# Optimization experiments

Measured on AMD Instinct MI355X. Metric: run time of the kernel, lower is better.

The kernel has to match this reference:

```python
import jax, jax.numpy as jnp
import numpy as np

HIDDEN = 768
HEADS = 12
HEAD_DIM = HIDDEN // HEADS


def setup_inputs() -> dict:
    key = jax.random.key(0)
    ks = jax.random.split(key, 6)
    B, N = 32, 577  # N = 1 CLS + 576 patches
    x = jax.random.normal(ks[0], (B, N, HIDDEN), dtype=jnp.float32)
    seg_bias = jax.random.uniform(ks[1], (B, N - 1), dtype=jnp.float32)
    w_qkv = jax.random.normal(ks[2], (HIDDEN, 3 * HIDDEN), dtype=jnp.float32) * 0.02
    b_qkv = jnp.zeros((3 * HIDDEN,), dtype=jnp.float32)
    w_proj = jax.random.normal(ks[3], (HIDDEN, HIDDEN), dtype=jnp.float32) * 0.02
    b_proj = jnp.zeros((HIDDEN,), dtype=jnp.float32)
    seg_scale = jnp.ones((), dtype=jnp.float32)
    return {"x": x, "seg_bias": seg_bias, "w_qkv": w_qkv, "b_qkv": b_qkv,
            "w_proj": w_proj, "b_proj": b_proj, "seg_scale": seg_scale}


def reference(x, seg_bias, w_qkv, b_qkv, w_proj, b_proj, seg_scale):
    B, N, _ = x.shape
    scale = HEAD_DIM ** -0.5
    qkv = x @ w_qkv + b_qkv                       # (B, N, 3*H*D)
    qkv = qkv.reshape(B, N, 3, HEADS, HEAD_DIM)
    q = qkv[:, :, 0].transpose(0, 2, 1, 3)        # (B, H, N, D)
    k = qkv[:, :, 1].transpose(0, 2, 1, 3)
    v = qkv[:, :, 2].transpose(0, 2, 1, 3)
    attn = jnp.einsum('bhqd,bhkd->bhqk', q, k) * scale  # (B, H, N, N)
    # additive seg bias on CLS-query row, patch keys only (cols 1:)
    bias = (seg_bias * seg_scale)[:, None, None, :]     # (B,1,1,N-1)
    attn = attn.at[:, :, 0:1, 1:].add(bias)
    attn = jax.nn.softmax(attn, axis=-1)
    out = jnp.einsum('bhqk,bhkd->bhqd', attn, v)        # (B, H, N, D)
    out = out.transpose(0, 2, 1, 3).reshape(B, N, HIDDEN)
    return out @ w_proj + b_proj
```

## Files before the change

kernel.cpp:

```cpp
#include <hip/hip_runtime.h>


typedef unsigned short bf16_t;
typedef __attribute__((ext_vector_type(8))) short short8;
typedef __attribute__((ext_vector_type(4))) short short4v;
typedef __attribute__((ext_vector_type(4))) float f32x4;

#define B_    32
#define N_    577
#define BN_   18464
#define HID_  768
#define NH_   12
#define HD_   64
#define QKVC_ 2304
#define NPAD_ 640
#define PB_LD 68

__device__ __forceinline__ bf16_t f2bf(float f) {
  union { float f; unsigned u; } x; x.f = f;
  unsigned r = x.u + 0x7fffu + ((x.u >> 16) & 1u);
  return (bf16_t)(r >> 16);
}

__device__ __forceinline__ unsigned cvt_pk_bf16(float a, float b) {
  unsigned r;
  asm("v_cvt_pk_bf16_f32 %0, %1, %2" : "=v"(r) : "v"(a), "v"(b));
  return r;
}

__global__ __launch_bounds__(256) void cast_kernel(const float* __restrict__ in,
                                                   bf16_t* __restrict__ out, int n4) {
  int i = blockIdx.x * 256 + threadIdx.x;
  if (i >= n4) return;
  float4 v = ((const float4*)in)[i];
  ushort4 o;
  o.x = f2bf(v.x); o.y = f2bf(v.y); o.z = f2bf(v.z); o.w = f2bf(v.w);
  ((ushort4*)out)[i] = o;
}

__global__ __launch_bounds__(256) void transpose_cast_kernel(const float* __restrict__ in,
                                                             bf16_t* __restrict__ out,
                                                             int R, int C) {
  __shared__ float tile[32][33];
  int c0 = blockIdx.x * 32, r0 = blockIdx.y * 32;
  int tx = threadIdx.x, ty = threadIdx.y;
  #pragma unroll
  for (int i = ty; i < 32; i += 8)
    tile[i][tx] = in[(size_t)(r0 + i) * C + c0 + tx];
  __syncthreads();
  #pragma unroll
  for (int i = ty; i < 32; i += 8)
    out[(size_t)(c0 + i) * R + r0 + tx] = f2bf(tile[tx][i]);
}

template <int OUT_BF16>
__global__ __launch_bounds__(256, 3) void gemm_bf16_kernel(
    const bf16_t* __restrict__ A,
    const bf16_t* __restrict__ Bt,
    const float* __restrict__ bias,
    void* __restrict__ Cout,
    int M, int Nc) {
  __shared__ bf16_t As[128 * 64];
  __shared__ bf16_t Bs[128 * 64];

  const int tid  = threadIdx.x;
  const int lane = tid & 63, w = tid >> 6;
  const int quad = lane >> 4, l16 = lane & 15;

  const int Mb = (M + 127) >> 7;
  const int Nb = Nc >> 7;
  const int np_full = Mb >> 3;
  const int rem = Mb - np_full * 8;
  int bid = blockIdx.x;
  int m_blk, n_blk;
  int body = np_full * 8 * Nb;
  if (bid < body) {
    int p = bid / (8 * Nb), local = bid % (8 * Nb);
    m_blk = p * 8 + (local & 7);
    n_blk = local >> 3;
  } else {
    int t = bid - body;
    m_blk = np_full * 8 + t % rem;
    n_blk = t / rem;
  }
  const int m0 = m_blk * 128, n0 = n_blk * 128;
  const int wm = (w >> 1) * 64, wn = (w & 1) * 64;

  f32x4 acc[4][4];
  #pragma unroll
  for (int i = 0; i < 4; ++i)
    #pragma unroll
    for (int j = 0; j < 4; ++j)
      acc[i][j] = (f32x4){0.f, 0.f, 0.f, 0.f};

  for (int kt = 0; kt < 768; kt += 64) {
    __syncthreads();
    #pragma unroll
    for (int it = 0; it < 4; ++it) {
      int gi = it * 256 + tid;
      int row = gi >> 3, chp = gi & 7;
      int ch = chp ^ (row & 7);
      int gm = m0 + row; if (gm >= M) gm = M - 1;
      __builtin_amdgcn_global_load_lds(
          (const __attribute__((address_space(1))) unsigned int*)(A + (size_t)gm * 768 + kt + ch * 8),
          (__attribute__((address_space(3))) unsigned int*)(As + gi * 8),
          16, 0, 0);
      int gn = n0 + row;
      __builtin_amdgcn_global_load_lds(
          (const __attribute__((address_space(1))) unsigned int*)(Bt + (size_t)gn * 768 + kt + ch * 8),
          (__attribute__((address_space(3))) unsigned int*)(Bs + gi * 8),
          16, 0, 0);
    }
    __syncthreads();

    #pragma unroll
    for (int ks = 0; ks < 2; ++ks) {
      short8 af[4], bfr[4];
      #pragma unroll
      for (int i = 0; i < 4; ++i) {
        int row = wm + i * 16 + l16;
        int c = ks * 4 + quad;
        af[i] = *(const short8*)(As + row * 64 + (c ^ (row & 7)) * 8);
      }
      #pragma unroll
      for (int j = 0; j < 4; ++j) {
        int row = wn + j * 16 + l16;
        int c = ks * 4 + quad;
        bfr[j] = *(const short8*)(Bs + row * 64 + (c ^ (row & 7)) * 8);
      }
      #pragma unroll
      for (int i = 0; i < 4; ++i)
        #pragma unroll
        for (int j = 0; j < 4; ++j)
          acc[i][j] = __builtin_amdgcn_mfma_f32_16x16x32_bf16(af[i], bfr[j], acc[i][j], 0, 0, 0);
    }
  }

  #pragma unroll
  for (int i = 0; i < 4; ++i) {
    int mrow_base = m0 + wm + i * 16 + quad * 4;
    #pragma unroll
    for (int j = 0; j < 4; ++j) {
      int col = n0 + wn + j * 16 + l16;
      float bs = bias[col];
      #pragma unroll
      for (int r = 0; r < 4; ++r) {
        int row = mrow_base + r;
        if (row < M) {
          float v = acc[i][j][r] + bs;
          if (OUT_BF16)
            ((bf16_t*)Cout)[(size_t)row * Nc + col] = f2bf(v);
          else
            ((float*)Cout)[(size_t)row * Nc + col] = v;
        }
      }
    }
  }
}

__global__ __launch_bounds__(256) void vt_kernel(const bf16_t* __restrict__ qkv,
                                                 bf16_t* __restrict__ vT) {
  const int t = blockIdx.x, h = blockIdx.y, b = blockIdx.z;
  const int tid = threadIdx.x;
  __shared__ bf16_t Ls[64 * 65];
  const int kv0 = t * 64;
  const bf16_t* Vp = qkv + (size_t)b * N_ * QKVC_ + 2 * HID_ + h * HD_;

  #pragma unroll
  for (int it = 0; it < 2; ++it) {
    int idx = it * 256 + tid;
    int row = idx >> 3, ch = idx & 7;
    int krow = kv0 + row; if (krow > N_ - 1) krow = N_ - 1;
    short8 v8 = *(const short8*)(Vp + (size_t)krow * QKVC_ + ch * 8);
    #pragma unroll
    for (int j = 0; j < 8; ++j)
      Ls[(ch * 8 + j) * 65 + row] = (bf16_t)v8[j];
  }
  __syncthreads();
  bf16_t* outp = vT + ((size_t)(b * NH_ + h) * HD_) * NPAD_;
  #pragma unroll
  for (int it = 0; it < 2; ++it) {
    int idx = it * 256 + tid;
    int d = idx >> 3, kc = idx & 7;
    short8 o8;
    #pragma unroll
    for (int j = 0; j < 8; ++j) {
      int p = kc * 8 + j;
      int ky = ((p & 3) << 4) | (p >> 2);
      o8[j] = (short)Ls[d * 65 + ky];
    }
    *(short8*)(outp + (size_t)d * NPAD_ + kv0 + kc * 8) = o8;
  }
}

__global__ __launch_bounds__(256) void attn_kernel(
    const bf16_t* __restrict__ qkv,
    const bf16_t* __restrict__ vT,
    const float* __restrict__ seg_bias,
    const float* __restrict__ seg_scale,
    bf16_t* __restrict__ out) {
  const int bid  = blockIdx.x;
  const int pair = bid % (B_ * NH_);
  const int qt   = bid / (B_ * NH_);
  const int h    = pair % NH_;
  const int b    = pair / NH_;
  const int tid = threadIdx.x;
  const int w = tid >> 6, lane = tid & 63;
  const int quad = lane >> 4, l16 = lane & 15;

  __shared__ bf16_t Ks[2][64 * 72];
  __shared__ bf16_t Vt[2][64 * 72];
  __shared__ bf16_t Pb[4][32 * PB_LD];

  const bf16_t* Qbase = qkv + (size_t)b * N_ * QKVC_ + h * HD_;
  const bf16_t* Kbase = Qbase + HID_;
  const bf16_t* Vtb   = vT + ((size_t)(b * NH_ + h) * HD_) * NPAD_;

  const int q0 = qt * 128 + w * 32;
  short8 qf[2][2];
  #pragma unroll
  for (int mi = 0; mi < 2; ++mi) {
    int qr = q0 + mi * 16 + l16;
    if (qr > N_ - 1) qr = N_ - 1;
    qf[mi][0] = *(const short8*)(Qbase + (size_t)qr * QKVC_ + quad * 8);
    qf[mi][1] = *(const short8*)(Qbase + (size_t)qr * QKVC_ + 32 + quad * 8);
  }
  const float qsc = 0.125f * 1.44269504f;
  #pragma unroll
  for (int mi = 0; mi < 2; ++mi)
    #pragma unroll
    for (int c = 0; c < 2; ++c)
      #pragma unroll
      for (int j = 0; j < 8; ++j) {
        unsigned u = ((unsigned)(unsigned short)qf[mi][c][j]) << 16;
        union { unsigned u; float f; } x; x.u = u;
        qf[mi][c][j] = (short)f2bf(x.f * qsc);
      }

  f32x4 o[2][4];
  float lsum[2][4];
  #pragma unroll
  for (int mi = 0; mi < 2; ++mi)
    #pragma unroll
    for (int j = 0; j < 4; ++j) {
      o[mi][j] = (f32x4){0.f, 0.f, 0.f, 0.f};
      lsum[mi][j] = 0.f;
    }

  const float ssl = seg_scale[0] * 1.44269504f;
  const bool bias_wave = (qt == 0 && w == 0);
  bf16_t* pw = Pb[w];

  const int srow = tid >> 3;
  const int sch  = tid & 7;

  short8 kpre[2], vpre[2];
  #pragma unroll
  for (int it = 0; it < 2; ++it) {
    int row = it * 32 + srow;
    int krow = row; if (krow > N_ - 1) krow = N_ - 1;
    kpre[it] = *(const short8*)(Kbase + (size_t)krow * QKVC_ + sch * 8);
    vpre[it] = *(const short8*)(Vtb + (size_t)row * NPAD_ + sch * 8);
  }
  #pragma unroll
  for (int it = 0; it < 2; ++it) {
    int row = it * 32 + srow;
    *(short8*)(&Ks[0][0] + row * 72 + sch * 8) = kpre[it];
    *(short8*)(&Vt[0][0] + row * 72 + sch * 8) = vpre[it];
  }
  __syncthreads();

  for (int t = 0; t < 10; ++t) {
    const int cur = t & 1;
    const int kv0 = t * 64;
    const bf16_t* ks = &Ks[cur][0];
    const bf16_t* vt = &Vt[cur][0];

    if (t < 9) {
      const int kv1 = kv0 + 64;
      #pragma unroll
      for (int it = 0; it < 2; ++it) {
        int row = it * 32 + srow;
        int krow = kv1 + row; if (krow > N_ - 1) krow = N_ - 1;
        kpre[it] = *(const short8*)(Kbase + (size_t)krow * QKVC_ + sch * 8);
        vpre[it] = *(const short8*)(Vtb + (size_t)row * NPAD_ + kv1 + sch * 8);
      }
    }

    f32x4 s[2][4];
    #pragma unroll
    for (int mi = 0; mi < 2; ++mi)
      #pragma unroll
      for (int sub = 0; sub < 4; ++sub)
        s[mi][sub] = (f32x4){0.f, 0.f, 0.f, 0.f};
    #pragma unroll
    for (int sub = 0; sub < 4; ++sub) {
      short8 k0 = *(const short8*)(ks + (sub * 16 + l16) * 72 + quad * 8);
      short8 k1 = *(const short8*)(ks + (sub * 16 + l16) * 72 + 32 + quad * 8);
      #pragma unroll
      for (int mi = 0; mi < 2; ++mi) {
        s[mi][sub] = __builtin_amdgcn_mfma_f32_16x16x32_bf16(qf[mi][0], k0, s[mi][sub], 0, 0, 0);
        s[mi][sub] = __builtin_amdgcn_mfma_f32_16x16x32_bf16(qf[mi][1], k1, s[mi][sub], 0, 0, 0);
      }
    }

    if (bias_wave && quad == 0) {
      #pragma unroll
      for (int sub = 0; sub < 4; ++sub) {
        int key = kv0 + sub * 16 + l16;
        if (key >= 1 && key < N_)
          s[0][sub][0] += seg_bias[b * (N_ - 1) + key - 1] * ssl;
      }
    }

    #pragma unroll
    for (int mi = 0; mi < 2; ++mi)
      #pragma unroll
      for (int r = 0; r < 4; ++r) {
        float p[4];
        #pragma unroll
        for (int sub = 0; sub < 4; ++sub) {
          float v = __builtin_amdgcn_exp2f(s[mi][sub][r]);
          if (t == 9) {
            int key = kv0 + sub * 16 + l16;
            if (key >= N_) v = 0.f;
          }
          lsum[mi][r] += v;
          p[sub] = v;
        }
        uint2 pk;
        pk.x = cvt_pk_bf16(p[0], p[1]);
        pk.y = cvt_pk_bf16(p[2], p[3]);
        *(uint2*)(pw + (mi * 16 + quad * 4 + r) * PB_LD + l16 * 4) = pk;
      }

    #pragma unroll
    for (int mi = 0; mi < 2; ++mi) {
      const bf16_t* pr = pw + (mi * 16 + l16) * PB_LD + quad * 8;
      union { short8 v; short4v h[2]; } pa0, pa1;
      pa0.h[0] = *(const short4v*)(pr);
      pa0.h[1] = *(const short4v*)(pr + 4);
      pa1.h[0] = *(const short4v*)(pr + 32);
      pa1.h[1] = *(const short4v*)(pr + 36);
      #pragma unroll
      for (int ds = 0; ds < 4; ++ds) {
        short8 vb0 = *(const short8*)(vt + (ds * 16 + l16) * 72 + quad * 8);
        short8 vb1 = *(const short8*)(vt + (ds * 16 + l16) * 72 + 32 + quad * 8);
        o[mi][ds] = __builtin_amdgcn_mfma_f32_16x16x32_bf16(pa0.v, vb0, o[mi][ds], 0, 0, 0);
        o[mi][ds] = __builtin_amdgcn_mfma_f32_16x16x32_bf16(pa1.v, vb1, o[mi][ds], 0, 0, 0);
      }
    }

    if (t < 9) {
      bf16_t* ksn = &Ks[1 - cur][0];
      bf16_t* vtn = &Vt[1 - cur][0];
      #pragma unroll
      for (int it = 0; it < 2; ++it) {
        int row = it * 32 + srow;
        *(short8*)(ksn + row * 72 + sch * 8) = kpre[it];
        *(short8*)(vtn + row * 72 + sch * 8) = vpre[it];
      }
    }
    __syncthreads();
  }

  #pragma unroll
  for (int mi = 0; mi < 2; ++mi)
    #pragma unroll
    for (int r = 0; r < 4; ++r) {
      float l = lsum[mi][r];
      #pragma unroll
      for (int off = 1; off < 16; off <<= 1)
        l += __shfl_xor(l, off);
      float inv = 1.0f / l;
      int row = q0 + mi * 16 + quad * 4 + r;
      if (row < N_) {
        size_t base = ((size_t)b * N_ + row) * HID_ + h * HD_;
        #pragma unroll
        for (int ds = 0; ds < 4; ++ds)
          out[base + ds * 16 + l16] = f2bf(o[mi][ds][r] * inv);
      }
    }
}

extern "C" void kernel_launch(void* const* d_in, const int* in_sizes, int n_in,
                              void* d_out, int out_size, void* d_ws, size_t ws_size,
                              hipStream_t stream) {
  const float* x         = (const float*)d_in[0];
  const float* seg_bias  = (const float*)d_in[1];
  const float* w_qkv     = (const float*)d_in[2];
  const float* b_qkv     = (const float*)d_in[3];
  const float* w_proj    = (const float*)d_in[4];
  const float* b_proj    = (const float*)d_in[5];
  const float* seg_scale = (const float*)d_in[6];

  char* ws = (char*)d_ws;
  bf16_t* xb     = (bf16_t*)ws;
  bf16_t* wqkvT  = (bf16_t*)(ws + 28360704);
  bf16_t* wprojT = (bf16_t*)(ws + 31899648);
  bf16_t* qkvb   = (bf16_t*)(ws + 33079296);
  bf16_t* vT     = (bf16_t*)(ws + 118161408);
  bf16_t* attnb  = xb;

  cast_kernel<<<(BN_ * HID_ / 4) / 256, 256, 0, stream>>>(x, xb, BN_ * HID_ / 4);
  dim3 tb(32, 8);
  transpose_cast_kernel<<<dim3(QKVC_ / 32, HID_ / 32), tb, 0, stream>>>(w_qkv, wqkvT, HID_, QKVC_);
  transpose_cast_kernel<<<dim3(HID_ / 32, HID_ / 32), tb, 0, stream>>>(w_proj, wprojT, HID_, HID_);

  gemm_bf16_kernel<1><<<145 * (QKVC_ / 128), 256, 0, stream>>>(
      xb, wqkvT, b_qkv, (void*)qkvb, BN_, QKVC_);

  vt_kernel<<<dim3(10, NH_, B_), 256, 0, stream>>>(qkvb, vT);

  attn_kernel<<<5 * NH_ * B_, 256, 0, stream>>>(qkvb, vT, seg_bias, seg_scale, attnb);

  gemm_bf16_kernel<0><<<145 * (HID_ / 128), 256, 0, stream>>>(
      attnb, wprojT, b_proj, d_out, BN_, HID_);
}
```

Measured before the change: 325.1 us.

## Use async global-to-LDS loads with XOR swizzle and MFMA row sums in attention

The attention kernel now stages K and V tiles with global_load_lds straight into swizzled, unpadded LDS buffers and synchronises with explicit waitcnt and barriers instead of register staging. This removes the register round trip and bank-conflict padding. The softmax denominator is now accumulated by an MFMA against a ones vector, replacing per-element adds and the cross-lane shuffle reduction. The last, mostly padded tile is peeled so only its single valid key is computed. Wave priority hints are also added around the MFMA sections. The risk is fragile hand synchronisation via the vmcnt counts, plus extra MFMA work for the row sums.

```diff
diff --git a/kernel.cpp b/kernel.cpp
--- a/kernel.cpp
+++ b/kernel.cpp
@@ -207,14 +207,30 @@
   const int tid = threadIdx.x;
   const int w = tid >> 6, lane = tid & 63;
   const int quad = lane >> 4, l16 = lane & 15;
-
-  __shared__ bf16_t Ks[2][64 * 72];
-  __shared__ bf16_t Vt[2][64 * 72];
-  __shared__ bf16_t Pb[4][32 * PB_LD];
+  const int xsw = l16 & 7;
+
+  __shared__ __align__(16) bf16_t Ks[2][64 * 64];
+  __shared__ __align__(16) bf16_t Vt[2][64 * 64];
+  __shared__ __align__(16) bf16_t Pb[4][32 * PB_LD];
 
   const bf16_t* Qbase = qkv + (size_t)b * N_ * QKVC_ + h * HD_;
   const bf16_t* Kbase = Qbase + HID_;
   const bf16_t* Vtb   = vT + ((size_t)(b * NH_ + h) * HD_) * NPAD_;
+
+  const float ssl = seg_scale[0] * 1.44269504f;
+
+  #pragma unroll
+  for (int it = 0; it < 2; ++it) {
+    int gi = it * 256 + tid;
+    int row = gi >> 3;
+    int ch = (gi & 7) ^ (row & 7);
+    __builtin_amdgcn_global_load_lds(
+        (const __attribute__((address_space(1))) unsigned int*)(Kbase + (size_t)row * QKVC_ + ch * 8),
+        (__attribute__((address_space(3))) unsigned int*)(&Ks[0][0] + gi * 8), 16, 0, 0);
+    __builtin_amdgcn_global_load_lds(
+        (const __attribute__((address_space(1))) unsigned int*)(Vtb + (size_t)row * NPAD_ + ch * 8),
+        (__attribute__((address_space(3))) unsigned int*)(&Vt[0][0] + gi * 8), 16, 0, 0);
+  }
 
   const int q0 = qt * 128 + w * 32;
   short8 qf[2][2];
@@ -237,78 +253,76 @@
         qf[mi][c][j] = (short)f2bf(x.f * qsc);
       }
 
+  const f32x4 z4 = {0.f, 0.f, 0.f, 0.f};
   f32x4 o[2][4];
-  float lsum[2][4];
-  #pragma unroll
-  for (int mi = 0; mi < 2; ++mi)
-    #pragma unroll
-    for (int j = 0; j < 4; ++j) {
-      o[mi][j] = (f32x4){0.f, 0.f, 0.f, 0.f};
-      lsum[mi][j] = 0.f;
-    }
-
-  const float ssl = seg_scale[0] * 1.44269504f;
+  f32x4 ls[2];
+  #pragma unroll
+  for (int mi = 0; mi < 2; ++mi) {
+    ls[mi] = z4;
+    #pragma unroll
+    for (int j = 0; j < 4; ++j) o[mi][j] = z4;
+  }
+
+  short8 ones;
+  #pragma unroll
+  for (int j = 0; j < 8; ++j) ones[j] = (short)0x3F80;
+
   const bool bias_wave = (qt == 0 && w == 0);
   bf16_t* pw = Pb[w];
 
-  const int srow = tid >> 3;
-  const int sch  = tid & 7;
-
-  short8 kpre[2], vpre[2];
-  #pragma unroll
-  for (int it = 0; it < 2; ++it) {
-    int row = it * 32 + srow;
-    int krow = row; if (krow > N_ - 1) krow = N_ - 1;
-    kpre[it] = *(const short8*)(Kbase + (size_t)krow * QKVC_ + sch * 8);
-    vpre[it] = *(const short8*)(Vtb + (size_t)row * NPAD_ + sch * 8);
-  }
-  #pragma unroll
-  for (int it = 0; it < 2; ++it) {
-    int row = it * 32 + srow;
-    *(short8*)(&Ks[0][0] + row * 72 + sch * 8) = kpre[it];
-    *(short8*)(&Vt[0][0] + row * 72 + sch * 8) = vpre[it];
-  }
-  __syncthreads();
-
-  for (int t = 0; t < 10; ++t) {
+  for (int t = 0; t < 9; ++t) {
     const int cur = t & 1;
-    const int kv0 = t * 64;
+
+    __builtin_amdgcn_s_barrier();
+    __builtin_amdgcn_sched_barrier(0);
+
+    {
+      const int kv1 = (t + 1) * 64;
+      bf16_t* ksn = &Ks[1 - cur][0];
+      bf16_t* vtn = &Vt[1 - cur][0];
+      #pragma unroll
+      for (int it = 0; it < 2; ++it) {
+        int gi = it * 256 + tid;
+        int row = gi >> 3;
+        int ch = (gi & 7) ^ (row & 7);
+        int krow = kv1 + row; if (krow > N_ - 1) krow = N_ - 1;
+        __builtin_amdgcn_global_load_lds(
+            (const __attribute__((address_space(1))) unsigned int*)(Kbase + (size_t)krow * QKVC_ + ch * 8),
+            (__attribute__((address_space(3))) unsigned int*)(ksn + gi * 8), 16, 0, 0);
+        __builtin_amdgcn_global_load_lds(
+            (const __attribute__((address_space(1))) unsigned int*)(Vtb + (size_t)row * NPAD_ + kv1 + ch * 8),
+            (__attribute__((address_space(3))) unsigned int*)(vtn + gi * 8), 16, 0, 0);
+      }
+    }
+
+    asm volatile("s_waitcnt vmcnt(4)" ::: "memory");
+    __builtin_amdgcn_sched_barrier(0);
+    __builtin_amdgcn_s_barrier();
+    __builtin_amdgcn_sched_barrier(0);
+
     const bf16_t* ks = &Ks[cur][0];
     const bf16_t* vt = &Vt[cur][0];
 
-    if (t < 9) {
-      const int kv1 = kv0 + 64;
-      #pragma unroll
-      for (int it = 0; it < 2; ++it) {
-        int row = it * 32 + srow;
-        int krow = kv1 + row; if (krow > N_ - 1) krow = N_ - 1;
-        kpre[it] = *(const short8*)(Kbase + (size_t)krow * QKVC_ + sch * 8);
-        vpre[it] = *(const short8*)(Vtb + (size_t)row * NPAD_ + kv1 + sch * 8);
-      }
-    }
-
     f32x4 s[2][4];
-    #pragma unroll
-    for (int mi = 0; mi < 2; ++mi)
-      #pragma unroll
-      for (int sub = 0; sub < 4; ++sub)
-        s[mi][sub] = (f32x4){0.f, 0.f, 0.f, 0.f};
+    __builtin_amdgcn_s_setprio(1);
     #pragma unroll
     for (int sub = 0; sub < 4; ++sub) {
-      short8 k0 = *(const short8*)(ks + (sub * 16 + l16) * 72 + quad * 8);
-      short8 k1 = *(const short8*)(ks + (sub * 16 + l16) * 72 + 32 + quad * 8);
+      short8 k0 = *(const short8*)(ks + (sub * 16 + l16) * 64 + (quad ^ xsw) * 8);
+      short8 k1 = *(const short8*)(ks + (sub * 16 + l16) * 64 + ((4 + quad) ^ xsw) * 8);
       #pragma unroll
       for (int mi = 0; mi < 2; ++mi) {
-        s[mi][sub] = __builtin_amdgcn_mfma_f32_16x16x32_bf16(qf[mi][0], k0, s[mi][sub], 0, 0, 0);
+        s[mi][sub] = __builtin_amdgcn_mfma_f32_16x16x32_bf16(qf[mi][0], k0, z4, 0, 0, 0);
         s[mi][sub] = __builtin_amdgcn_mfma_f32_16x16x32_bf16(qf[mi][1], k1, s[mi][sub], 0, 0, 0);
       }
     }
+    __builtin_amdgcn_s_setprio(0);
 
     if (bias_wave && quad == 0) {
+      const int kv0 = t * 64;
       #pragma unroll
       for (int sub = 0; sub < 4; ++sub) {
         int key = kv0 + sub * 16 + l16;
-        if (key >= 1 && key < N_)
+        if (key >= 1)
           s[0][sub][0] += seg_bias[b * (N_ - 1) + key - 1] * ssl;
       }
     }
@@ -317,62 +331,89 @@
     for (int mi = 0; mi < 2; ++mi)
       #pragma unroll
       for (int r = 0; r < 4; ++r) {
-        float p[4];
-        #pragma unroll
-        for (int sub = 0; sub < 4; ++sub) {
-          float v = __builtin_amdgcn_exp2f(s[mi][sub][r]);
-          if (t == 9) {
-            int key = kv0 + sub * 16 + l16;
-            if (key >= N_) v = 0.f;
-          }
-          lsum[mi][r] += v;
-          p[sub] = v;
-        }
+        float p0 = __builtin_amdgcn_exp2f(s[mi][0][r]);
+        float p1 = __builtin_amdgcn_exp2f(s[mi][1][r]);
+        float p2 = __builtin_amdgcn_exp2f(s[mi][2][r]);
+        float p3 = __builtin_amdgcn_exp2f(s[mi][3][r]);
         uint2 pk;
-        pk.x = cvt_pk_bf16(p[0], p[1]);
-        pk.y = cvt_pk_bf16(p[2], p[3]);
+        pk.x = cvt_pk_bf16(p0, p1);
+        pk.y = cvt_pk_bf16(p2, p3);
         *(uint2*)(pw + (mi * 16 + quad * 4 + r) * PB_LD + l16 * 4) = pk;
       }
 
     #pragma unroll
     for (int mi = 0; mi < 2; ++mi) {
       const bf16_t* pr = pw + (mi * 16 + l16) * PB_LD + quad * 8;
-      union { short8 v; short4v h[2]; } pa0, pa1;
-      pa0.h[0] = *(const short4v*)(pr);
-      pa0.h[1] = *(const short4v*)(pr + 4);
-      pa1.h[0] = *(const short4v*)(pr + 32);
-      pa1.h[1] = *(const short4v*)(pr + 36);
+      union { short8 v; short4v hv[2]; } pa0, pa1;
+      pa0.hv[0] = *(const short4v*)(pr);
+      pa0.hv[1] = *(const short4v*)(pr + 4);
+      pa1.hv[0] = *(const short4v*)(pr + 32);
+      pa1.hv[1] = *(const short4v*)(pr + 36);
+      __builtin_amdgcn_s_setprio(1);
+      ls[mi] = __builtin_amdgcn_mfma_f32_16x16x32_bf16(pa0.v, ones, ls[mi], 0, 0, 0);
+      ls[mi] = __builtin_amdgcn_mfma_f32_16x16x32_bf16(pa1.v, ones, ls[mi], 0, 0, 0);
       #pragma unroll
       for (int ds = 0; ds < 4; ++ds) {
-        short8 vb0 = *(const short8*)(vt + (ds * 16 + l16) * 72 + quad * 8);
-        short8 vb1 = *(const short8*)(vt + (ds * 16 + l16) * 72 + 32 + quad * 8);
+        short8 vb0 = *(const short8*)(vt + (ds * 16 + l16) * 64 + (quad ^ xsw) * 8);
+        short8 vb1 = *(const short8*)(vt + (ds * 16 + l16) * 64 + ((4 + quad) ^ xsw) * 8);
         o[mi][ds] = __builtin_amdgcn_mfma_f32_16x16x32_bf16(pa0.v, vb0, o[mi][ds], 0, 0, 0);
         o[mi][ds] = __builtin_amdgcn_mfma_f32_16x16x32_bf16(pa1.v, vb1, o[mi][ds], 0, 0, 0);
       }
-    }
-
-    if (t < 9) {
-      bf16_t* ksn = &Ks[1 - cur][0];
-      bf16_t* vtn = &Vt[1 - cur][0];
-      #pragma unroll
-      for (int it = 0; it < 2; ++it) {
-        int row = it * 32 + srow;
-        *(short8*)(ksn + row * 72 + sch * 8) = kpre[it];
-        *(short8*)(vtn + row * 72 + sch * 8) = vpre[it];
-      }
-    }
-    __syncthreads();
+      __builtin_amdgcn_s_setprio(0);
+    }
+  }
+
+  {
+    asm volatile("s_waitcnt vmcnt(0)" ::: "memory");
+    __builtin_amdgcn_sched_barrier(0);
+    __builtin_amdgcn_s_barrier();
+    __builtin_amdgcn_sched_barrier(0);
+
+    const bf16_t* ks = &Ks[1][0];
+    const bf16_t* vt = &Vt[1][0];
+
+    short8 k0 = *(const short8*)(ks + l16 * 64 + (quad ^ xsw) * 8);
+    short8 k1 = *(const short8*)(ks + l16 * 64 + ((4 + quad) ^ xsw) * 8);
+    f32x4 s9[2];
+    #pragma unroll
+    for (int mi = 0; mi < 2; ++mi) {
+      s9[mi] = __builtin_amdgcn_mfma_f32_16x16x32_bf16(qf[mi][0], k0, z4, 0, 0, 0);
+      s9[mi] = __builtin_amdgcn_mfma_f32_16x16x32_bf16(qf[mi][1], k1, s9[mi], 0, 0, 0);
+    }
+    if (bias_wave && quad == 0 && l16 == 0)
+      s9[0][0] += seg_bias[b * (N_ - 1) + (N_ - 2)] * ssl;
+
+    #pragma unroll
+    for (int mi = 0; mi < 2; ++mi)
+      #pragma unroll
+      for (int r = 0; r < 4; ++r) {
+        float p0 = (l16 == 0) ? __builtin_amdgcn_exp2f(s9[mi][r]) : 0.f;
+        uint2 pk;
+        pk.x = cvt_pk_bf16(p0, 0.f);
+        pk.y = 0u;
+        *(uint2*)(pw + (mi * 16 + quad * 4 + r) * PB_LD + l16 * 4) = pk;
+      }
+
+    #pragma unroll
+    for (int mi = 0; mi < 2; ++mi) {
+      const bf16_t* pr = pw + (mi * 16 + l16) * PB_LD + quad * 8;
+      union { short8 v; short4v hv[2]; } pa0;
+      pa0.hv[0] = *(const short4v*)(pr);
+      pa0.hv[1] = *(const short4v*)(pr + 4);
+      ls[mi] = __builtin_amdgcn_mfma_f32_16x16x32_bf16(pa0.v, ones, ls[mi], 0, 0, 0);
+      #pragma unroll
+      for (int ds = 0; ds < 4; ++ds) {
+        short8 vb0 = *(const short8*)(vt + (ds * 16 + l16) * 64 + (quad ^ xsw) * 8);
+        o[mi][ds] = __builtin_amdgcn_mfma_f32_16x16x32_bf16(pa0.v, vb0, o[mi][ds], 0, 0, 0);
+      }
+    }
   }
 
   #pragma unroll
   for (int mi = 0; mi < 2; ++mi)
     #pragma unroll
     for (int r = 0; r < 4; ++r) {
-      float l = lsum[mi][r];
-      #pragma unroll
-      for (int off = 1; off < 16; off <<= 1)
-        l += __shfl_xor(l, off);
-      float inv = 1.0f / l;
+      float inv = 1.0f / ls[mi][r];
       int row = q0 + mi * 16 + quad * 4 + r;
       if (row < N_) {
         size_t base = ((size_t)b * N_ + row) * HID_ + h * HD_;
```

Measured after the change: 324.3 us. About the same (-0.3%).
